# Kernel tuning notes

Measured on AMD Instinct MI355X. Metric: run time of the kernel, lower is better.

Reference implementation:

```python
import jax, jax.numpy as jnp
from jax import lax
import numpy as np

D = 512        # d_model
F = 128        # raw feature dim
MS = 1024      # logic (service) nodes
NP_ = 16384    # physical nodes
EL = 4096      # logic edges
EP = 131072    # phys edges
SRC = 0        # source_node_idx
NEG = -1e9


def _gnn(feats, edge_index, Win, Wout, N):
    row, col = edge_index
    h = jax.nn.relu(feats @ Win)                                  # [N, D]
    agg = jax.ops.segment_sum(h[row], col, num_segments=N)        # [N, D]
    return jax.nn.relu((h + agg) @ Wout)


def _bfs_hop(edge_index, N, src, iters=16):
    # BFS hop distance from src (bounded Bellman-Ford relaxation)
    row, col = edge_index
    big = jnp.int32(N)
    dist = jnp.full((N,), big, jnp.int32).at[src].set(0)
    def body(_, d):
        cand = jnp.minimum(d[row] + 1, big)
        upd = jax.ops.segment_min(cand, col, num_segments=N)
        return jnp.minimum(d, upd)
    return lax.fori_loop(0, iters, body, dist)


def _forward(logic_feats, phys_feats, Ws_in, Ws_out, Wp_in, Wp_out,
             sA1, sA2, pA1, pA2, Wq, Wk, Wc1, bc1, wc2,
             logic_edge_index, phys_edge_index, actions, static_mask, topo_order):
    Np = phys_feats.shape[0]
    cloud = Np - 1                                                # cloud_node_idx = -1
    h_s = _gnn(logic_feats, logic_edge_index, Ws_in, Ws_out, logic_feats.shape[0])
    h_p = _gnn(phys_feats, phys_edge_index, Wp_in, Wp_out, Np)
    # task-specific residual adapters
    h_s = h_s + jax.nn.relu(h_s @ sA1) @ sA2
    h_p = h_p + jax.nn.relu(h_p @ pA1) @ pA2
    metric = _bfs_hop(phys_edge_index, Np, SRC)                   # [Np] int32
    q_all = (h_s @ Wq) / jnp.sqrt(jnp.float32(D))                 # [Ms, D]
    K = h_p @ Wk                                                  # [Np, D]
    acts = actions.astype(jnp.int32)

    def step(state, i):
        visited, last, logp_sum, ent_sum, switches, relax = state
        base = static_mask[i]                                     # [Np] bool
        # cloud_sticky branch
        sticky = jnp.zeros_like(base).at[cloud].set(base[cloud])
        # forbid_return (allow_stay keeps `last`)
        forbid = visited.at[last].set(False)
        allowed_n = base & (~forbid) & (metric >= metric[last])   # metric_non_decreasing
        allowed = jnp.where(last == cloud, sticky, allowed_n)
        any_a = allowed.any()
        # relaxation fallback: stay -> cloud -> base
        fb_stay = jnp.zeros_like(base).at[last].set(True)
        fb_cloud = jnp.zeros_like(base).at[cloud].set(True)
        fallback = jnp.where(base[last], fb_stay, jnp.where(base[cloud], fb_cloud, base))
        allowed = jnp.where(any_a, allowed, fallback)
        # actor: masked categorical over physical nodes
        logits = K @ q_all[i]                                     # [Np]
        logp_all = jax.nn.log_softmax(jnp.where(allowed, logits, NEG))
        p = jnp.exp(logp_all)
        ent = -jnp.sum(p * logp_all)
        a = acts[i]
        ne = a != last
        visited = visited.at[last].set(visited[last] | ne)
        last = jnp.where(ne, a, last)
        return (visited, last, logp_sum + logp_all[a], ent_sum + ent,
                switches + ne.astype(jnp.int32), relax + (~any_a).astype(jnp.int32)), None

    init = (jnp.zeros((Np,), bool), jnp.int32(SRC),
            jnp.float32(0.0), jnp.float32(0.0), jnp.int32(0), jnp.int32(0))
    (visited, last, logp_sum, ent_sum, switches, relax), _ = lax.scan(
        step, init, topo_order.astype(jnp.int32))
    # value head
    pooled = jnp.concatenate([h_s.mean(0), h_p.mean(0)])          # [2D]
    value = jax.nn.relu(pooled @ Wc1 + bc1) @ wc2                 # scalar
    return jnp.stack([logp_sum, ent_sum, value])


def setup_inputs() -> dict:
    key = jax.random.key(0)
    ks = jax.random.split(key, 20)
    s = 0.05
    def w(k, shape):
        return jax.random.normal(k, shape, jnp.float32) * s
    return {
        "logic_edge_index": jax.random.randint(ks[0], (2, EL), 0, MS, jnp.int32),
        "logic_feats": jax.random.normal(ks[1], (MS, F), jnp.float32),
        "phys_edge_index": jax.random.randint(ks[2], (2, EP), 0, NP_, jnp.int32),
        "phys_feats": jax.random.normal(ks[3], (NP_, F), jnp.float32),
        "actions": jax.random.randint(ks[4], (MS,), 0, NP_, jnp.int32),
        "static_mask": jnp.ones((MS, NP_), bool),
        "topo_order": jnp.arange(MS, dtype=jnp.int32),
        "Ws_in": w(ks[5], (F, D)), "Ws_out": w(ks[6], (D, D)),
        "Wp_in": w(ks[7], (F, D)), "Wp_out": w(ks[8], (D, D)),
        "sA1": w(ks[9], (D, D)), "sA2": w(ks[10], (D, D)),
        "pA1": w(ks[11], (D, D)), "pA2": w(ks[12], (D, D)),
        "Wq": w(ks[13], (D, D)), "Wk": w(ks[14], (D, D)),
        "Wc1": w(ks[15], (2 * D, D)),
        "bc1": jnp.zeros((D,), jnp.float32),
        "wc2": w(ks[16], (D,)),
    }


def reference(logic_edge_index, logic_feats, phys_edge_index, phys_feats,
              actions, static_mask, topo_order,
              Ws_in, Ws_out, Wp_in, Wp_out, sA1, sA2, pA1, pA2,
              Wq, Wk, Wc1, bc1, wc2):
    return _forward(logic_feats, phys_feats, Ws_in, Ws_out, Wp_in, Wp_out,
                    sA1, sA2, pA1, pA2, Wq, Wk, Wc1, bc1, wc2,
                    logic_edge_index, phys_edge_index, actions, static_mask, topo_order)
```

## Files before the change

kernel.cpp:

```cpp
#include <hip/hip_runtime.h>
#include <cstdint>
#include <cstddef>

typedef __bf16 bf16_t;
typedef bf16_t bf16x8 __attribute__((ext_vector_type(8)));
typedef bf16_t bf16x4v __attribute__((ext_vector_type(4)));
typedef float f32x4 __attribute__((ext_vector_type(4)));

#define NEGV (-1e9f)

#define GLDS(gp, lp) __builtin_amdgcn_global_load_lds( \
    (const __attribute__((address_space(1))) void*)(gp), \
    (__attribute__((address_space(3))) void*)(lp), 16, 0, 0)

struct PrepArgs {
    const float* w512src[8]; bf16_t* w512dst[8];
    const float* w128src[2]; bf16_t* w128dst[2];
    const float* logicF; const float* physF;
    bf16_t* featsSb; bf16_t* featsPb;
    const int* mask; uint32_t* bits;
    int* cntC; int* cntR; int* cntL; int* firstL; int* dist;
    float* pooled; float* hacc;
};

__global__ __launch_bounds__(256)
void k_prep(PrepArgs p) {
    __shared__ float tb[64][65];
    const int b = blockIdx.x, tid = threadIdx.x;
    if (b < 544) {
        const float* src; bf16_t* dst; int K, tile;
        if (b < 512) { src = p.w512src[b >> 6]; dst = p.w512dst[b >> 6]; K = 512; tile = b & 63; }
        else { int bb = b - 512; src = p.w128src[bb >> 4]; dst = p.w128dst[bb >> 4]; K = 128; tile = bb & 15; }
        const int N = 512;
        int kt = tile >> 3, tc = tile & 7;
        int cx = tid & 63, ry = tid >> 6;
#pragma unroll
        for (int q = 0; q < 16; ++q) {
            int r = q * 4 + ry;
            tb[r][cx] = src[(size_t)(kt * 64 + r) * N + tc * 64 + cx];
        }
        __syncthreads();
#pragma unroll
        for (int q = 0; q < 16; ++q) {
            int r2 = q * 4 + ry;
            dst[(size_t)(tc * 64 + r2) * K + kt * 64 + cx] = (bf16_t)tb[cx][r2];
        }
    } else if (b < 672) {
        size_t e0 = (size_t)(b - 544) * 1024 + tid * 4;
        float4 v = *(const float4*)(p.logicF + e0);
        bf16x4v o; o[0]=(bf16_t)v.x; o[1]=(bf16_t)v.y; o[2]=(bf16_t)v.z; o[3]=(bf16_t)v.w;
        *(bf16x4v*)(p.featsSb + e0) = o;
    } else if (b < 2720) {
        size_t e0 = (size_t)(b - 672) * 1024 + tid * 4;
        float4 v = *(const float4*)(p.physF + e0);
        bf16x4v o; o[0]=(bf16_t)v.x; o[1]=(bf16_t)v.y; o[2]=(bf16_t)v.z; o[3]=(bf16_t)v.w;
        *(bf16x4v*)(p.featsPb + e0) = o;
    } else if (b < 2784) {
        int gid = (b - 2720) * 256 + tid;
        p.cntC[gid] = 0; p.cntR[gid] = 0; p.firstL[gid] = 0x7fffffff;
        p.dist[gid] = (gid == 0) ? 0 : 16384;
        if (gid < 1024) { p.cntL[gid] = 0; p.pooled[gid] = 0.0f; }
        if (gid < 512) p.hacc[gid] = 0.0f;
    } else {
        size_t w = (size_t)(b - 2784) * 256 + tid;
        const int4* q4 = (const int4*)(p.mask + w * 32);
        uint32_t bb = 0;
#pragma unroll
        for (int q = 0; q < 8; ++q) {
            int4 v = q4[q];
            bb |= (v.x != 0 ? 1u : 0u) << (q * 4);
            bb |= (v.y != 0 ? 1u : 0u) << (q * 4 + 1);
            bb |= (v.z != 0 ? 1u : 0u) << (q * 4 + 2);
            bb |= (v.w != 0 ? 1u : 0u) << (q * 4 + 3);
        }
        p.bits[w] = bb;
    }
}

__global__ void k_hist3(const int* __restrict__ rowP, const int* __restrict__ colP,
                        const int* __restrict__ rowL, const int* __restrict__ colL,
                        int* cntC, int* cntR, int* cntL, int EP, int EL,
                        const int* __restrict__ topo, const int* __restrict__ acts,
                        int* __restrict__ lastArr, int* __restrict__ firstL) {
    int b = blockIdx.x;
    if (b < 1040) {
        int e = b * 256 + threadIdx.x;
        if (e < EP) atomicAdd(&cntC[colP[e]], 1);
        else if (e < 2 * EP) atomicAdd(&cntR[rowP[e - EP]], 1);
        else if (e < 2 * EP + EL) atomicAdd(&cntL[colL[e - 2 * EP]], 1);
    } else {
        int s = (b - 1040) * 256 + threadIdx.x;
        int last = (s == 0) ? 0 : acts[topo[s - 1]];
        lastArr[s] = last;
        int a = acts[topo[s]];
        if (a != last) atomicMin(&firstL[last], s);
    }
}

__global__ __launch_bounds__(256)
void k_scan3(int* cntC, int* offC, int* curC,
             int* cntR, int* offR, int* curR,
             int* cntL, int* offL, int* curL) {
    __shared__ int ss[256];
    int tid = threadIdx.x;
    const int* cnt; int* off; int* cur; int n;
    if (blockIdx.x == 0)      { cnt = cntC; off = offC; cur = curC; n = 16384; }
    else if (blockIdx.x == 1) { cnt = cntR; off = offR; cur = curR; n = 16384; }
    else                      { cnt = cntL; off = offL; cur = curL; n = 1024; }
    int chunk = n / 256, base = tid * chunk, s = 0;
    for (int i = 0; i < chunk; ++i) s += cnt[base + i];
    ss[tid] = s; __syncthreads();
    for (int d = 1; d < 256; d <<= 1) {
        int v = (tid >= d) ? ss[tid - d] : 0;
        __syncthreads(); ss[tid] += v; __syncthreads();
    }
    int run = (tid == 0) ? 0 : ss[tid - 1];
    for (int i = 0; i < chunk; ++i) { off[base + i] = run; cur[base + i] = run; run += cnt[base + i]; }
    if (tid == 255) off[n] = run;
}

__global__ void k_scatter3(const int* __restrict__ rowP, const int* __restrict__ colP,
                           const int* __restrict__ rowL, const int* __restrict__ colL,
                           int* curC, int* curR, int* curL,
                           int* erowCP, int* ecolRP, int* erowL, int EP, int EL) {
    int e = blockIdx.x * 256 + threadIdx.x;
    if (e < EP) {
        int c = colP[e]; int q = atomicAdd(&curC[c], 1); erowCP[q] = rowP[e];
    } else if (e < 2 * EP) {
        int e2 = e - EP;
        int c = rowP[e2]; int q = atomicAdd(&curR[c], 1); ecolRP[q] = colP[e2];
    } else if (e < 2 * EP + EL) {
        int e3 = e - 2 * EP;
        int c = colL[e3]; int q = atomicAdd(&curL[c], 1); erowL[q] = rowL[e3];
    }
}

__global__ __launch_bounds__(256)
void k_bfs_level(const int* __restrict__ offR, const int* __restrict__ ecol,
                 int* __restrict__ dist, int lev) {
    int j = blockIdx.x * 256 + threadIdx.x;
    if (dist[j] != lev) return;
    int e0 = offR[j], e1 = offR[j + 1];
    for (int e = e0; e < e1; ++e) {
        int v = ecol[e];
        if (dist[v] == 16384) dist[v] = lev + 1;
    }
}

__global__ __launch_bounds__(256)
void k_fmpack(const int* __restrict__ firstL, const int* __restrict__ dist, int* __restrict__ fm) {
    int j = blockIdx.x * 256 + threadIdx.x;
    int fl = firstL[j]; if (fl > 0xFFFF) fl = 0xFFFF;
    fm[j] = (fl << 16) | dist[j];
}

struct GemmDesc { const bf16_t* A; const bf16_t* B; const bf16_t* Cin; bf16_t* O;
                  int N; int K; float scale; int relu; };
struct GemmPair { GemmDesc d0; GemmDesc d1; int split; };

__global__ __launch_bounds__(256)
void gemm_mfma(GemmPair args) {
    __shared__ bf16_t As[2][128 * 32];
    __shared__ bf16_t Bs[2][128 * 32];
    const int inSet1 = (blockIdx.y >= args.split);
    const GemmDesc g = inSet1 ? args.d1 : args.d0;
    const int my = blockIdx.y - (inSet1 ? args.split : 0);
    const int m0 = my * 128, n0 = blockIdx.x * 128;
    const int tid = threadIdx.x, wave = tid >> 6, lane = tid & 63;
    const int wm = (wave >> 1) * 64, wn = (wave & 1) * 64;
    const int lr = lane & 15, lk = (lane >> 4) * 8;
    const int K = g.K;
    const int srr = wave * 16 + (lane >> 2);
    const int scb = (((lane & 3) ^ ((lane >> 2) & 3)) << 4);
    const char* Abase = (const char*)g.A + ((size_t)(m0 + srr) * K) * 2 + scb;
    const char* Bbase = (const char*)g.B + ((size_t)(n0 + srr) * K) * 2 + scb;
    const size_t rstep = (size_t)64 * K * 2;
    f32x4 acc[4][4] = {};

    auto stage = [&](int q, int k0) {
        const char* a0 = Abase + (size_t)k0 * 2;
        const char* b0 = Bbase + (size_t)k0 * 2;
        GLDS(a0,         &As[q][(wave * 16) * 32]);
        GLDS(a0 + rstep, &As[q][(64 + wave * 16) * 32]);
        GLDS(b0,         &Bs[q][(wave * 16) * 32]);
        GLDS(b0 + rstep, &Bs[q][(64 + wave * 16) * 32]);
    };

    stage(0, 0);
    asm volatile("s_waitcnt vmcnt(0)" ::: "memory");
    __syncthreads();
    const int nt = K >> 5;
    for (int t = 0; t < nt; ++t) {
        int cur = t & 1;
        if (t + 1 < nt) stage(cur ^ 1, (t + 1) << 5);
        bf16x8 af[4], bff[4];
#pragma unroll
        for (int mi = 0; mi < 4; ++mi) {
            int r = wm + mi * 16 + lr;
            int pb = r * 64 + ((lk * 2) ^ ((r & 3) << 4));
            af[mi] = *(const bf16x8*)((const char*)&As[cur][0] + pb);
        }
#pragma unroll
        for (int ni = 0; ni < 4; ++ni) {
            int r = wn + ni * 16 + lr;
            int pb = r * 64 + ((lk * 2) ^ ((r & 3) << 4));
            bff[ni] = *(const bf16x8*)((const char*)&Bs[cur][0] + pb);
        }
#pragma unroll
        for (int mi = 0; mi < 4; ++mi)
#pragma unroll
            for (int ni = 0; ni < 4; ++ni)
                acc[mi][ni] = __builtin_amdgcn_mfma_f32_16x16x32_bf16(af[mi], bff[ni], acc[mi][ni], 0, 0, 0);
        asm volatile("s_waitcnt vmcnt(0)" ::: "memory");
        __syncthreads();
    }
    const int rb = m0 + wm + (lane >> 4) * 4;
    const int cb = n0 + wn + lr;
#pragma unroll
    for (int mi = 0; mi < 4; ++mi)
#pragma unroll
        for (int ni = 0; ni < 4; ++ni)
#pragma unroll
            for (int r = 0; r < 4; ++r) {
                int row = rb + mi * 16 + r;
                int col = cb + ni * 16;
                size_t idx = (size_t)row * g.N + col;
                float v = acc[mi][ni][r] * g.scale;
                if (g.Cin) v += (float)g.Cin[idx];
                if (g.relu) v = fmaxf(v, 0.0f);
                g.O[idx] = (bf16_t)v;
            }
}

__global__ __launch_bounds__(256)
void k_spmm2(const bf16_t* __restrict__ HL, const int* __restrict__ offL, const int* __restrict__ erowL, bf16_t* __restrict__ XL,
             const bf16_t* __restrict__ HP, const int* __restrict__ offP, const int* __restrict__ erowP, bf16_t* __restrict__ XP) {
    int b = blockIdx.x;
    const bf16_t* H; const int* off; const int* erow; bf16_t* X; int c;
    int wib = threadIdx.x >> 6, lane = threadIdx.x & 63;
    if (b < 256) { H = HL; off = offL; erow = erowL; X = XL; c = b * 4 + wib; }
    else { b -= 256; H = HP; off = offP; erow = erowP; X = XP; c = b * 4 + wib; }
    int d0 = lane * 8;
    float acc[8] = {0,0,0,0,0,0,0,0};
    int e0 = off[c], e1 = off[c + 1];
    for (int e = e0; e < e1; ++e) {
        int r = erow[e];
        bf16x8 h = *(const bf16x8*)(H + (size_t)r * 512 + d0);
#pragma unroll
        for (int j = 0; j < 8; ++j) acc[j] += (float)h[j];
    }
    bf16x8 own = *(const bf16x8*)(H + (size_t)c * 512 + d0);
    bf16x8 o;
#pragma unroll
    for (int j = 0; j < 8; ++j) o[j] = (bf16_t)((float)own[j] + acc[j]);
    *(bf16x8*)(X + (size_t)c * 512 + d0) = o;
}

__global__ __launch_bounds__(256)
void k_scan2(const bf16_t* __restrict__ S, const uint32_t* __restrict__ bits,
             const int* __restrict__ fm, const int* __restrict__ topo,
             const int* __restrict__ acts, const int* __restrict__ lastA,
             float* __restrict__ slogp, float* __restrict__ sent) {
    const int NPn = 16384, cloud = NPn - 1;
    __shared__ float msh[256], zsh[256], wsh[256];
    __shared__ int ash[256];
    const int s = blockIdx.x, tid = threadIdx.x;
    const int i = topo[s], a = acts[i], last = lastA[s];
    const bf16_t* Srow = S + (size_t)i * NPn;
    const uint32_t* brow = bits + (size_t)i * 512;
    const int ml = fm[last] & 0xFFFF;
    const int baseCloud = (brow[511] >> 31) & 1;
    const int lic = (last == cloud);
    if (lic && baseCloud) {
        if (tid == 0) {
            float M = (float)Srow[cloud];
            slogp[s] = (a == cloud) ? 0.0f : (NEGV - M);
            sent[s] = 0.0f;
        }
        return;
    }
    float m = -3.4e38f, Z = 0.0f, W = 0.0f;
    int any = 0;
    if (!lic) {
        for (int c = 0; c < 8; ++c) {
            int j0 = c * 2048 + tid * 8;
            bf16x8 sv = *(const bf16x8*)(Srow + j0);
            uint32_t b8 = (brow[j0 >> 5] >> (j0 & 24)) & 0xFFu;
            int4 f0 = *(const int4*)(fm + j0);
            int4 f1 = *(const int4*)(fm + j0 + 4);
            int fj[8] = {f0.x, f0.y, f0.z, f0.w, f1.x, f1.y, f1.z, f1.w};
#pragma unroll
            for (int q = 0; q < 8; ++q) {
                int j = j0 + q;
                bool alw = ((b8 >> q) & 1) && ((fj[q] & 0xFFFF) >= ml)
                           && (j == last || (((unsigned)fj[q]) >> 16) >= (unsigned)s);
                if (alw) {
                    any = 1;
                    float l = (float)sv[q];
                    if (l > m) {
                        float d = m - l, ce = expf(d);
                        W = ce * (W + d * Z);
                        Z = ce * Z + 1.0f;
                        m = l;
                    } else {
                        float t = l - m, e = expf(t);
                        Z += e; W += t * e;
                    }
                }
            }
        }
    }
    msh[tid] = m; zsh[tid] = Z; wsh[tid] = W; ash[tid] = any;
    __syncthreads();
    for (int st = 128; st > 0; st >>= 1) {
        if (tid < st) {
            float m1 = msh[tid], Z1 = zsh[tid], W1 = wsh[tid];
            float m2 = msh[tid + st], Z2 = zsh[tid + st], W2 = wsh[tid + st];
            float M2 = fmaxf(m1, m2);
            float e1 = expf(m1 - M2), e2 = expf(m2 - M2);
            zsh[tid] = e1 * Z1 + e2 * Z2;
            wsh[tid] = e1 * (W1 + (m1 - M2) * Z1) + e2 * (W2 + (m2 - M2) * Z2);
            msh[tid] = M2;
            ash[tid] |= ash[tid + st];
        }
        __syncthreads();
    }
    if (tid != 0) return;
    if (ash[0]) {
        float M = msh[0], Zt = zsh[0], Wt = wsh[0];
        float logZ = logf(Zt);
        int fa = fm[a];
        bool alwa = ((brow[a >> 5] >> (a & 31)) & 1) && ((fa & 0xFFFF) >= ml)
                    && (a == last || (((unsigned)fa) >> 16) >= (unsigned)s);
        float la = alwa ? (float)Srow[a] : NEGV;
        slogp[s] = la - M - logZ;
        sent[s] = logZ - Wt / Zt;
        return;
    }
    int baseLast = (brow[last >> 5] >> (last & 31)) & 1;
    if (baseLast) { float M = (float)Srow[last]; slogp[s] = (a == last) ? 0.0f : (NEGV - M); sent[s] = 0.0f; return; }
    if (baseCloud) { float M = (float)Srow[cloud]; slogp[s] = (a == cloud) ? 0.0f : (NEGV - M); sent[s] = 0.0f; return; }
    float mm = -3.4e38f, ZZ = 0.0f, WW = 0.0f;
    for (int j = 0; j < NPn; ++j) {
        if ((brow[j >> 5] >> (j & 31)) & 1) {
            float l = (float)Srow[j];
            if (l > mm) { float d = mm - l, ce = expf(d); WW = ce * (WW + d * ZZ); ZZ = ce * ZZ + 1.0f; mm = l; }
            else { float t = l - mm, e = expf(t); ZZ += e; WW += t * e; }
        }
    }
    if (ZZ == 0.0f) { slogp[s] = -logf((float)NPn); sent[s] = logf((float)NPn); return; }
    float logZ = logf(ZZ);
    int ba = (brow[a >> 5] >> (a & 31)) & 1;
    float la = ba ? (float)Srow[a] : NEGV;
    slogp[s] = la - mm - logZ;
    sent[s] = logZ - WW / ZZ;
}

__global__ __launch_bounds__(256)
void k_pool2(const bf16_t* __restrict__ HL, const bf16_t* __restrict__ HP, float* __restrict__ pooled) {
    int b = blockIdx.x, tid = threadIdx.x;
    const bf16_t* H; float* dst; int R, bb, ng; float inv;
    if (b < 16) { H = HL; dst = pooled; R = 1024; inv = 1.0f / 1024.0f; bb = b; ng = 16; }
    else { H = HP; dst = pooled + 512; R = 16384; inv = 1.0f / 16384.0f; bb = b - 16; ng = 128; }
    float a0 = 0, a1 = 0;
    for (int r = bb; r < R; r += ng) {
        a0 += (float)H[(size_t)r * 512 + tid];
        a1 += (float)H[(size_t)r * 512 + tid + 256];
    }
    atomicAdd(&dst[tid], a0 * inv);
    atomicAdd(&dst[tid + 256], a1 * inv);
}

__global__ __launch_bounds__(256)
void k_vpart(const float* __restrict__ pooled, const float* __restrict__ Wc1, float* __restrict__ hacc) {
    __shared__ float pk[128];
    int b = blockIdx.x, tid = threadIdx.x;
    int k0 = b * 128;
    if (tid < 128) pk[tid] = pooled[k0 + tid];
    __syncthreads();
    float a0 = 0, a1 = 0;
    for (int kk = 0; kk < 128; ++kk) {
        float pv = pk[kk];
        const float* wr = Wc1 + (size_t)(k0 + kk) * 512;
        a0 += pv * wr[tid];
        a1 += pv * wr[tid + 256];
    }
    atomicAdd(&hacc[tid], a0);
    atomicAdd(&hacc[tid + 256], a1);
}

__global__ __launch_bounds__(256)
void k_epilogue(const float* __restrict__ slogp, const float* __restrict__ sent,
                const float* __restrict__ hacc, const float* __restrict__ bc1,
                const float* __restrict__ wc2, float* __restrict__ out) {
    __shared__ float s1[256], s2[256], s3[256];
    int tid = threadIdx.x;
    float a = 0, b = 0;
    for (int k = tid; k < 1024; k += 256) { a += slogp[k]; b += sent[k]; }
    float v = fmaxf(hacc[tid] + bc1[tid], 0.0f) * wc2[tid]
            + fmaxf(hacc[tid + 256] + bc1[tid + 256], 0.0f) * wc2[tid + 256];
    s1[tid] = a; s2[tid] = b; s3[tid] = v;
    __syncthreads();
    for (int st = 128; st > 0; st >>= 1) {
        if (tid < st) { s1[tid] += s1[tid + st]; s2[tid] += s2[tid + st]; s3[tid] += s3[tid + st]; }
        __syncthreads();
    }
    if (tid == 0) { out[0] = s1[0]; out[1] = s2[0]; out[2] = s3[0]; }
}

extern "C" void kernel_launch(void* const* d_in, const int* in_sizes, int n_in,
                              void* d_out, int out_size, void* d_ws, size_t ws_size,
                              hipStream_t stream) {
    (void)n_in; (void)out_size; (void)ws_size; (void)in_sizes;
    const int MS = 1024, NP = 16384, EL = 4096, EP = 131072, D = 512;

    const int* logicE = (const int*)d_in[0];
    const float* logicF = (const float*)d_in[1];
    const int* physE = (const int*)d_in[2];
    const float* physF = (const float*)d_in[3];
    const int* acts = (const int*)d_in[4];
    const int* mask = (const int*)d_in[5];
    const int* topo = (const int*)d_in[6];
    const float* Ws_in = (const float*)d_in[7];
    const float* Ws_out = (const float*)d_in[8];
    const float* Wp_in = (const float*)d_in[9];
    const float* Wp_out = (const float*)d_in[10];
    const float* sA1 = (const float*)d_in[11];
    const float* sA2 = (const float*)d_in[12];
    const float* pA1 = (const float*)d_in[13];
    const float* pA2 = (const float*)d_in[14];
    const float* Wq = (const float*)d_in[15];
    const float* Wk = (const float*)d_in[16];
    const float* Wc1 = (const float*)d_in[17];
    const float* bc1 = (const float*)d_in[18];
    const float* wc2 = (const float*)d_in[19];
    float* out = (float*)d_out;

    char* wsb = (char*)d_ws;
    size_t off = 0;
    auto alloc = [&](size_t bytes) -> void* {
        off = (off + 255) & ~(size_t)255;
        void* p = wsb + off; off += bytes; return p;
    };

    bf16_t* S_bf    = (bf16_t*)alloc((size_t)MS * NP * 2);
    bf16_t* PB0     = (bf16_t*)alloc((size_t)NP * D * 2);
    bf16_t* PB1     = (bf16_t*)alloc((size_t)NP * D * 2);
    bf16_t* PB2     = (bf16_t*)alloc((size_t)NP * D * 2);
    bf16_t* LB0     = (bf16_t*)alloc((size_t)MS * D * 2);
    bf16_t* LB1     = (bf16_t*)alloc((size_t)MS * D * 2);
    bf16_t* LB2     = (bf16_t*)alloc((size_t)MS * D * 2);
    bf16_t* featsSb = (bf16_t*)alloc((size_t)MS * 128 * 2);
    bf16_t* featsPb = (bf16_t*)alloc((size_t)NP * 128 * 2);
    bf16_t* WsinT   = (bf16_t*)alloc(512 * 128 * 2);
    bf16_t* WpinT   = (bf16_t*)alloc(512 * 128 * 2);
    bf16_t* WsoutT  = (bf16_t*)alloc(512 * 512 * 2);
    bf16_t* sA1T    = (bf16_t*)alloc(512 * 512 * 2);
    bf16_t* sA2T    = (bf16_t*)alloc(512 * 512 * 2);
    bf16_t* WqT     = (bf16_t*)alloc(512 * 512 * 2);
    bf16_t* WpoutT  = (bf16_t*)alloc(512 * 512 * 2);
    bf16_t* pA1T    = (bf16_t*)alloc(512 * 512 * 2);
    bf16_t* pA2T    = (bf16_t*)alloc(512 * 512 * 2);
    bf16_t* WkT     = (bf16_t*)alloc(512 * 512 * 2);
    uint32_t* bits = (uint32_t*)alloc((size_t)MS * NP / 8);
    int* cntC  = (int*)alloc(NP * 4);
    int* offC  = (int*)alloc((NP + 1) * 4);
    int* curC  = (int*)alloc(NP * 4);
    int* cntR  = (int*)alloc(NP * 4);
    int* offR  = (int*)alloc((NP + 1) * 4);
    int* curR  = (int*)alloc(NP * 4);
    int* cntL  = (int*)alloc(MS * 4);
    int* offL  = (int*)alloc((MS + 1) * 4);
    int* curL  = (int*)alloc(MS * 4);
    int* erowCP = (int*)alloc(EP * 4);
    int* ecolRP = (int*)alloc(EP * 4);
    int* erowL  = (int*)alloc(EL * 4);
    int* firstL = (int*)alloc(NP * 4);
    int* lastA  = (int*)alloc(MS * 4);
    int* dist   = (int*)alloc(NP * 4);
    int* fm     = (int*)alloc(NP * 4);
    float* slogp = (float*)alloc(MS * 4);
    float* sentb = (float*)alloc(MS * 4);
    float* pooled = (float*)alloc(1024 * 4);
    float* hacc   = (float*)alloc(512 * 4);

    const int* rowP = physE;  const int* colP = physE + EP;
    const int* rowL = logicE; const int* colL = logicE + EL;

    {
        PrepArgs p;
        const float* s512[8] = {Ws_out, sA1, sA2, Wq, Wp_out, pA1, pA2, Wk};
        bf16_t* d512[8] = {WsoutT, sA1T, sA2T, WqT, WpoutT, pA1T, pA2T, WkT};
        for (int q = 0; q < 8; ++q) { p.w512src[q] = s512[q]; p.w512dst[q] = d512[q]; }
        p.w128src[0] = Ws_in; p.w128dst[0] = WsinT;
        p.w128src[1] = Wp_in; p.w128dst[1] = WpinT;
        p.logicF = logicF; p.physF = physF; p.featsSb = featsSb; p.featsPb = featsPb;
        p.mask = mask; p.bits = bits;
        p.cntC = cntC; p.cntR = cntR; p.cntL = cntL; p.firstL = firstL; p.dist = dist;
        p.pooled = pooled; p.hacc = hacc;
        hipLaunchKernelGGL(k_prep, dim3(4832), dim3(256), 0, stream, p);
    }
    hipLaunchKernelGGL(k_hist3, dim3(1044), dim3(256), 0, stream,
                       rowP, colP, rowL, colL, cntC, cntR, cntL, EP, EL,
                       topo, acts, lastA, firstL);
    hipLaunchKernelGGL(k_scan3, dim3(3), dim3(256), 0, stream,
                       cntC, offC, curC, cntR, offR, curR, cntL, offL, curL);
    hipLaunchKernelGGL(k_scatter3, dim3((2 * EP + EL) / 256), dim3(256), 0, stream,
                       rowP, colP, rowL, colL, curC, curR, curL, erowCP, ecolRP, erowL, EP, EL);
    for (int lev = 0; lev < 16; ++lev)
        hipLaunchKernelGGL(k_bfs_level, dim3(64), dim3(256), 0, stream, offR, ecolRP, dist, lev);
    hipLaunchKernelGGL(k_fmpack, dim3(64), dim3(256), 0, stream, firstL, dist, fm);

    auto gemm2 = [&](const bf16_t* A0, const bf16_t* B0, const bf16_t* C0, bf16_t* O0, float sc0,
                     const bf16_t* A1, const bf16_t* B1, const bf16_t* C1, bf16_t* O1, float sc1,
                     int K, int relu) {
        GemmPair gp;
        gp.d0 = {A0, B0, C0, O0, 512, K, sc0, relu};
        gp.d1 = {A1, B1, C1, O1, 512, K, sc1, relu};
        gp.split = 8;
        hipLaunchKernelGGL(gemm_mfma, dim3(4, 136), dim3(256), 0, stream, gp);
    };

    gemm2(featsSb, WsinT, nullptr, LB0, 1.0f, featsPb, WpinT, nullptr, PB0, 1.0f, 128, 1);
    hipLaunchKernelGGL(k_spmm2, dim3(256 + 4096), dim3(256), 0, stream,
                       LB0, offL, erowL, LB1, PB0, offC, erowCP, PB1);
    gemm2(LB1, WsoutT, nullptr, LB0, 1.0f, PB1, WpoutT, nullptr, PB0, 1.0f, 512, 1);
    gemm2(LB0, sA1T, nullptr, LB1, 1.0f, PB0, pA1T, nullptr, PB1, 1.0f, 512, 1);
    gemm2(LB1, sA2T, LB0, LB2, 1.0f, PB1, pA2T, PB0, PB2, 1.0f, 512, 0);
    hipLaunchKernelGGL(k_pool2, dim3(144), dim3(256), 0, stream, LB2, PB2, pooled);
    gemm2(LB2, WqT, nullptr, LB1, 0.044194173824159216f, PB2, WkT, nullptr, PB1, 1.0f, 512, 0);
    {
        GemmPair gp;
        gp.d0 = {LB1, PB1, nullptr, S_bf, NP, 512, 1.0f, 0};
        gp.d1 = gp.d0;
        gp.split = 1000;
        hipLaunchKernelGGL(gemm_mfma, dim3(128, 8), dim3(256), 0, stream, gp);
    }
    hipLaunchKernelGGL(k_scan2, dim3(MS), dim3(256), 0, stream,
                       S_bf, bits, fm, topo, acts, lastA, slogp, sentb);
    hipLaunchKernelGGL(k_vpart, dim3(8), dim3(256), 0, stream, pooled, Wc1, hacc);
    hipLaunchKernelGGL(k_epilogue, dim3(1), dim3(256), 0, stream, slogp, sentb, hacc, bc1, wc2, out);
}
```

Measured before the change: 393.4 us.

## Fuse the four dense GEMM stages and pooling into one LDS-resident row-tile kernel

Replaces four separate paired GEMM launches (Wout, adapter A1, adapter A2 with residual, Wq/Wk projection) and the pooling kernel with one kernel. Each block keeps a 64-row tile in shared memory across all four stages and streams the weights from global memory, with the pooled mean computed from the LDS tile. This removes global round trips of the intermediate activations and several launches. In exchange it uses only 272 blocks at one block per CU with large LDS use, re-reads the weights for every tile, and has limited latency hiding.

```diff
diff --git a/kernel.cpp b/kernel.cpp
--- a/kernel.cpp
+++ b/kernel.cpp
@@ -232,6 +232,93 @@
             }
 }
 
+struct FusedSide { const bf16_t* X; const bf16_t* W1; const bf16_t* W2; const bf16_t* W3; const bf16_t* W4;
+                   bf16_t* OUT; float* pool; float scale; float pinv; };
+struct FusedPair { FusedSide s0; FusedSide s1; int split; };
+
+__global__ __launch_bounds__(256, 1)
+void k_fused_chain(FusedPair fp) {
+    __shared__ bf16_t bufA[64][520];
+    __shared__ bf16_t bufB[64][520];
+    const int tid = threadIdx.x, wave = tid >> 6, lane = tid & 63;
+    const int lr = lane & 15, lkq = lane >> 4;
+    const int wc = wave * 128;
+    const int inS1 = (blockIdx.x >= fp.split);
+    const FusedSide sd = inS1 ? fp.s1 : fp.s0;
+    const int mb = blockIdx.x - (inS1 ? fp.split : 0);
+    const size_t row0 = (size_t)mb * 64;
+
+    const bf16_t* Xt = sd.X + row0 * 512;
+#pragma unroll
+    for (int q = 0; q < 16; ++q) {
+        int flat = (q * 256 + tid) * 8;
+        bf16x8 v = *(const bf16x8*)(Xt + flat);
+        *(bf16x8*)&bufA[flat >> 9][flat & 511] = v;
+    }
+    __syncthreads();
+
+    auto run_stage = [&](const bf16_t (*src)[520], const bf16_t* WT, bf16_t (*dst)[520], int mode) {
+        f32x4 acc[4][8] = {};
+        bf16x8 bc[8];
+#pragma unroll
+        for (int ni = 0; ni < 8; ++ni)
+            bc[ni] = *(const bf16x8*)(WT + (size_t)(wc + ni * 16 + lr) * 512 + lkq * 8);
+        for (int st = 0; st < 16; ++st) {
+            const int kk = st * 32;
+            bf16x8 bn[8];
+            if (st < 15) {
+#pragma unroll
+                for (int ni = 0; ni < 8; ++ni)
+                    bn[ni] = *(const bf16x8*)(WT + (size_t)(wc + ni * 16 + lr) * 512 + kk + 32 + lkq * 8);
+            }
+            bf16x8 af[4];
+#pragma unroll
+            for (int mi = 0; mi < 4; ++mi)
+                af[mi] = *(const bf16x8*)&src[mi * 16 + lr][kk + lkq * 8];
+#pragma unroll
+            for (int mi = 0; mi < 4; ++mi)
+#pragma unroll
+                for (int ni = 0; ni < 8; ++ni)
+                    acc[mi][ni] = __builtin_amdgcn_mfma_f32_16x16x32_bf16(af[mi], bc[ni], acc[mi][ni], 0, 0, 0);
+            if (st < 15) {
+#pragma unroll
+                for (int ni = 0; ni < 8; ++ni) bc[ni] = bn[ni];
+            }
+        }
+#pragma unroll
+        for (int mi = 0; mi < 4; ++mi)
+#pragma unroll
+            for (int ni = 0; ni < 8; ++ni)
+#pragma unroll
+                for (int r = 0; r < 4; ++r) {
+                    int row = mi * 16 + lkq * 4 + r;
+                    int col = wc + ni * 16 + lr;
+                    float v = acc[mi][ni][r];
+                    if (mode == 0) {
+                        dst[row][col] = (bf16_t)fmaxf(v, 0.0f);
+                    } else if (mode == 2) {
+                        v += (float)bufB[row][col];
+                        bufB[row][col] = (bf16_t)v;
+                    } else {
+                        sd.OUT[(row0 + row) * 512 + col] = (bf16_t)(v * sd.scale);
+                    }
+                }
+    };
+
+    run_stage(bufA, sd.W1, bufB, 0);   __syncthreads();
+    run_stage(bufB, sd.W2, bufA, 0);   __syncthreads();
+    run_stage(bufA, sd.W3, nullptr, 2); __syncthreads();
+    run_stage(bufB, sd.W4, nullptr, 3);
+
+    float s0 = 0.0f, s1 = 0.0f;
+    for (int r = 0; r < 64; ++r) {
+        s0 += (float)bufB[r][tid];
+        s1 += (float)bufB[r][tid + 256];
+    }
+    atomicAdd(sd.pool + tid, s0 * sd.pinv);
+    atomicAdd(sd.pool + tid + 256, s1 * sd.pinv);
+}
+
 __global__ __launch_bounds__(256)
 void k_spmm2(const bf16_t* __restrict__ HL, const int* __restrict__ offL, const int* __restrict__ erowL, bf16_t* __restrict__ XL,
              const bf16_t* __restrict__ HP, const int* __restrict__ offP, const int* __restrict__ erowP, bf16_t* __restrict__ XP) {
@@ -354,21 +441,6 @@
     float la = ba ? (float)Srow[a] : NEGV;
     slogp[s] = la - mm - logZ;
     sent[s] = logZ - WW / ZZ;
-}
-
-__global__ __launch_bounds__(256)
-void k_pool2(const bf16_t* __restrict__ HL, const bf16_t* __restrict__ HP, float* __restrict__ pooled) {
-    int b = blockIdx.x, tid = threadIdx.x;
-    const bf16_t* H; float* dst; int R, bb, ng; float inv;
-    if (b < 16) { H = HL; dst = pooled; R = 1024; inv = 1.0f / 1024.0f; bb = b; ng = 16; }
-    else { H = HP; dst = pooled + 512; R = 16384; inv = 1.0f / 16384.0f; bb = b - 16; ng = 128; }
-    float a0 = 0, a1 = 0;
-    for (int r = bb; r < R; r += ng) {
-        a0 += (float)H[(size_t)r * 512 + tid];
-        a1 += (float)H[(size_t)r * 512 + tid + 256];
-    }
-    atomicAdd(&dst[tid], a0 * inv);
-    atomicAdd(&dst[tid + 256], a1 * inv);
 }
 
 __global__ __launch_bounds__(256)
@@ -461,7 +533,7 @@
     bf16_t* WpoutT  = (bf16_t*)alloc(512 * 512 * 2);
     bf16_t* pA1T    = (bf16_t*)alloc(512 * 512 * 2);
     bf16_t* pA2T    = (bf16_t*)alloc(512 * 512 * 2);
-    bf16_t* WkT     = (bf16_t*)alloc(512 * 512 * 2);
+    bf16_t* WkT    = (bf16_t*)alloc(512 * 512 * 2);
     uint32_t* bits = (uint32_t*)alloc((size_t)MS * NP / 8);
     int* cntC  = (int*)alloc(NP * 4);
     int* offC  = (int*)alloc((NP + 1) * 4);
@@ -511,27 +583,25 @@
         hipLaunchKernelGGL(k_bfs_level, dim3(64), dim3(256), 0, stream, offR, ecolRP, dist, lev);
     hipLaunchKernelGGL(k_fmpack, dim3(64), dim3(256), 0, stream, firstL, dist, fm);
 
-    auto gemm2 = [&](const bf16_t* A0, const bf16_t* B0, const bf16_t* C0, bf16_t* O0, float sc0,
-                     const bf16_t* A1, const bf16_t* B1, const bf16_t* C1, bf16_t* O1, float sc1,
-                     int K, int relu) {
+    {
         GemmPair gp;
-        gp.d0 = {A0, B0, C0, O0, 512, K, sc0, relu};
-        gp.d1 = {A1, B1, C1, O1, 512, K, sc1, relu};
+        gp.d0 = {featsSb, WsinT, nullptr, LB0, 512, 128, 1.0f, 1};
+        gp.d1 = {featsPb, WpinT, nullptr, PB0, 512, 128, 1.0f, 1};
         gp.split = 8;
         hipLaunchKernelGGL(gemm_mfma, dim3(4, 136), dim3(256), 0, stream, gp);
-    };
-
-    gemm2(featsSb, WsinT, nullptr, LB0, 1.0f, featsPb, WpinT, nullptr, PB0, 1.0f, 128, 1);
+    }
     hipLaunchKernelGGL(k_spmm2, dim3(256 + 4096), dim3(256), 0, stream,
                        LB0, offL, erowL, LB1, PB0, offC, erowCP, PB1);
-    gemm2(LB1, WsoutT, nullptr, LB0, 1.0f, PB1, WpoutT, nullptr, PB0, 1.0f, 512, 1);
-    gemm2(LB0, sA1T, nullptr, LB1, 1.0f, PB0, pA1T, nullptr, PB1, 1.0f, 512, 1);
-    gemm2(LB1, sA2T, LB0, LB2, 1.0f, PB1, pA2T, PB0, PB2, 1.0f, 512, 0);
-    hipLaunchKernelGGL(k_pool2, dim3(144), dim3(256), 0, stream, LB2, PB2, pooled);
-    gemm2(LB2, WqT, nullptr, LB1, 0.044194173824159216f, PB2, WkT, nullptr, PB1, 1.0f, 512, 0);
+    {
+        FusedPair fp;
+        fp.s0 = {LB1, WsoutT, sA1T, sA2T, WqT, LB0, pooled,       0.044194173824159216f, 1.0f / 1024.0f};
+        fp.s1 = {PB1, WpoutT, pA1T, pA2T, WkT, PB0, pooled + 512, 1.0f,                  1.0f / 16384.0f};
+        fp.split = 16;
+        hipLaunchKernelGGL(k_fused_chain, dim3(272), dim3(256), 0, stream, fp);
+    }
     {
         GemmPair gp;
-        gp.d0 = {LB1, PB1, nullptr, S_bf, NP, 512, 1.0f, 0};
+        gp.d0 = {LB0, PB0, nullptr, S_bf, NP, 512, 1.0f, 0};
         gp.d1 = gp.d0;
         gp.split = 1000;
         hipLaunchKernelGGL(gemm_mfma, dim3(128, 8), dim3(256), 0, stream, gp);
```

New measurement: 398.2 us. No clear change (+1.2%).
